# Kernel optimization log

Hardware: AMD Instinct MI355X
Metric: run time of the kernel (lower is better)

## Reference

```python
import math
import jax, jax.numpy as jnp
import numpy as np

B, S, E, H = 4, 2048, 1024, 16
D = E // H


def setup_inputs() -> dict:
    key = jax.random.key(0)
    k1, k2, k3 = jax.random.split(key, 3)
    return {
        "hidden_state": jax.random.normal(k1, (B, S, E), dtype=jnp.float32),
        "attention_mask": jnp.zeros((B, 1, 1, S), dtype=jnp.float32),
        "W_attn": jax.random.normal(k2, (E, 3 * E), dtype=jnp.float32) * 0.02,
        "b_attn": jnp.zeros((3 * E,), dtype=jnp.float32),
        "W_proj": jax.random.normal(k3, (E, E), dtype=jnp.float32) * 0.02,
        "b_proj": jnp.zeros((E,), dtype=jnp.float32),
    }


def reference(hidden_state, attention_mask, W_attn, b_attn, W_proj, b_proj):
    b, s, e = hidden_state.shape
    d = e // H
    # c_attn (HF Conv1D): x @ W + b -> [B,S,3E]
    x = hidden_state @ W_attn + b_attn
    q, k, v = jnp.split(x, 3, axis=-1)
    # split heads -> [B,H,S,D]
    q = q.reshape(b, s, H, d).transpose(0, 2, 1, 3)
    k = k.reshape(b, s, H, d).transpose(0, 2, 1, 3)
    v = v.reshape(b, s, H, d).transpose(0, 2, 1, 3)
    # scores [B,H,S,S]; scale=True divides by sqrt(d_head)
    w = jnp.einsum("bhqd,bhkd->bhqk", q, k) / math.sqrt(d)
    causal = jnp.tril(jnp.ones((s, s), dtype=w.dtype))[None, None]
    w = w * causal + (-10000.0) * (1.0 - causal)
    w = w + attention_mask
    w = jax.nn.softmax(w, axis=-1)  # attn_dropout p=0 (eval)
    out = jnp.einsum("bhqk,bhkd->bhqd", w, v)
    # merge heads -> [B,S,E]
    out = out.transpose(0, 2, 1, 3).reshape(b, s, e)
    # c_proj; resid_dropout p=0 (eval)
    return out @ W_proj + b_proj
```

## Files before the change

### kernel.cpp

```cpp
#include <hip/hip_runtime.h>
#include <hip/hip_bf16.h>

typedef __attribute__((ext_vector_type(4))) float f32x4;
typedef __attribute__((ext_vector_type(8))) short bf16x8;

#define B_SZ  4
#define S_LEN 2048
#define EMB   1024
#define NH    16
#define DH    64
#define E3    3072
#define QKLD  2048
#define LOG2E 1.4426950408889634f
#define SC2   (0.125f * LOG2E)
#define MSTAT 14.0f

__device__ __forceinline__ void gload_lds16(const void* g, void* l) {
  __builtin_amdgcn_global_load_lds((const __attribute__((address_space(1))) void*)g,
                                   (__attribute__((address_space(3))) void*)l, 16, 0, 0);
}

__device__ __forceinline__ float bf2f(unsigned short u) {
  union { unsigned int i; float f; } c;
  c.i = (unsigned int)u << 16;
  return c.f;
}

__global__ void cvt_bf16_kernel(const float* __restrict__ in,
                                __hip_bfloat16* __restrict__ out, int n) {
  const int i = (blockIdx.x * 256 + threadIdx.x) * 4;
  if (i >= n) return;
  const float4 v = *(const float4*)(in + i);
  __align__(8) __hip_bfloat16 o[4];
  o[0] = __float2bfloat16(v.x); o[1] = __float2bfloat16(v.y);
  o[2] = __float2bfloat16(v.z); o[3] = __float2bfloat16(v.w);
  *(uint2*)(out + i) = *(const uint2*)o;
}

__global__ __launch_bounds__(256)
void transpose_cvt(const float* __restrict__ in, __hip_bfloat16* __restrict__ out,
                   int R, int C) {
  __shared__ float tile[32][33];
  const int tx = threadIdx.x & 31, ty = threadIdx.x >> 5;
  const int c = blockIdx.x * 32 + tx;
#pragma unroll
  for (int i = 0; i < 32; i += 8)
    tile[ty + i][tx] = in[(size_t)(blockIdx.y * 32 + ty + i) * C + c];
  __syncthreads();
  const int r2 = blockIdx.y * 32 + tx;
#pragma unroll
  for (int i = 0; i < 32; i += 8)
    out[(size_t)(blockIdx.x * 32 + ty + i) * R + r2] = __float2bfloat16(tile[tx][ty + i]);
}

#define SBAR() { __builtin_amdgcn_s_barrier(); __builtin_amdgcn_sched_barrier(0); }
#define VMCNT(N) asm volatile("s_waitcnt vmcnt(" #N ")" ::: "memory")

#define STG_A(T, H, BUF) { \
    const __hip_bfloat16* s_ = pA + (size_t)((H) * 128) * 1024 + (T) * 64; \
    gload_lds16(s_, (BUF) + (H) * 16384 + w * 1024 + lane * 16); \
    gload_lds16(s_ + 65536, (BUF) + (H) * 16384 + 8192 + w * 1024 + lane * 16); }

#define STG_B(T, H, BUF) { \
    const __hip_bfloat16* s_ = pB + (size_t)((H) * 128) * 1024 + (T) * 64; \
    gload_lds16(s_, (BUF) + (H) * 16384 + w * 1024 + lane * 16); \
    gload_lds16(s_ + 65536, (BUF) + (H) * 16384 + 8192 + w * 1024 + lane * 16); }

#define RD_A(BUF, MH) { _Pragma("unroll") for (int m_ = 0; m_ < 4; ++m_) { \
    a[m_][0] = *(const bf16x8*)((BUF) + arow + ((MH) * 64 + m_ * 16) * 128 + sw0); \
    a[m_][1] = *(const bf16x8*)((BUF) + arow + ((MH) * 64 + m_ * 16) * 128 + sw1); } }

#define RD_B(BUF, NH, BARR) { _Pragma("unroll") for (int n_ = 0; n_ < 2; ++n_) { \
    BARR[n_][0] = *(const bf16x8*)((BUF) + brow + ((NH) * 32 + n_ * 16) * 128 + sw0); \
    BARR[n_][1] = *(const bf16x8*)((BUF) + brow + ((NH) * 32 + n_ * 16) * 128 + sw1); } }

#define MQUAD(MH, NH, BARR) { __builtin_amdgcn_s_setprio(1); \
    _Pragma("unroll") for (int m_ = 0; m_ < 4; ++m_) \
    _Pragma("unroll") for (int n_ = 0; n_ < 2; ++n_) \
    _Pragma("unroll") for (int k_ = 0; k_ < 2; ++k_) \
      acc[(MH)*4+m_][(NH)*2+n_] = __builtin_amdgcn_mfma_f32_16x16x32_bf16( \
          a[m_][k_], BARR[n_][k_], acc[(MH)*4+m_][(NH)*2+n_], 0, 0, 0); \
    __builtin_amdgcn_s_setprio(0); }

template <int EPI>
__global__ __launch_bounds__(512, 2)
void gemm_8ph(const __hip_bfloat16* __restrict__ A, const __hip_bfloat16* __restrict__ BT,
              const float* __restrict__ bias, void* __restrict__ Cout,
              __hip_bfloat16* __restrict__ vt) {
  __shared__ __attribute__((aligned(16))) char lds[131072];
  char* const As0 = lds;
  char* const As1 = lds + 32768;
  char* const Bs0 = lds + 65536;
  char* const Bs1 = lds + 98304;

  const int tid = threadIdx.x;
  const int lane = tid & 63, w = tid >> 6;
  const int lr = lane & 15, lg = lane >> 4, lg4 = lg * 4;
  const int wm = w >> 2, wn = w & 3;
  const int m0 = blockIdx.x * 256, n0 = blockIdx.y * 256;

  const int srl = lane >> 3;
  const int scol = ((lane & 7) ^ srl) * 8;
  const __hip_bfloat16* pA = A + (size_t)(m0 + w * 8 + srl) * 1024 + scol;
  const __hip_bfloat16* pB = BT + (size_t)(n0 + w * 8 + srl) * 1024 + scol;

  const int sw0 = (lg ^ (lr & 7)) << 4;
  const int sw1 = sw0 ^ 0x40;
  const int arow = (wm * 128 + lr) * 128;
  const int brow = (wn * 64 + lr) * 128;

  f32x4 acc[8][4] = {};
  bf16x8 a[4][2], b0[2][2], b1[2][2];

  STG_A(0, 0, As0); STG_B(0, 0, Bs0); STG_A(0, 1, As0); STG_B(0, 1, Bs0); STG_A(1, 0, As1);
  VMCNT(2);
  SBAR();

  auto iter = [&](int t0, bool more) {
    RD_A(As0, 0); RD_B(Bs0, 0, b0);
    STG_B(t0 + 1, 0, Bs1);
    SBAR(); MQUAD(0, 0, b0); SBAR();
    RD_B(Bs0, 1, b1);
    STG_A(t0 + 1, 1, As1);
    SBAR(); MQUAD(0, 1, b1); SBAR();
    RD_A(As0, 1); RD_B(Bs0, 0, b0);
    STG_B(t0 + 1, 1, Bs1);
    SBAR(); MQUAD(1, 0, b0); SBAR();
    RD_B(Bs0, 1, b1);
    if (more) { STG_A(t0 + 2, 0, As0); VMCNT(2); } else { VMCNT(0); }
    SBAR(); MQUAD(1, 1, b1); SBAR();
    RD_A(As1, 0); RD_B(Bs1, 0, b0);
    if (more) STG_B(t0 + 2, 0, Bs0);
    SBAR(); MQUAD(0, 0, b0); SBAR();
    RD_B(Bs1, 1, b1);
    if (more) STG_A(t0 + 2, 1, As0);
    SBAR(); MQUAD(0, 1, b1); SBAR();
    RD_A(As1, 1); RD_B(Bs1, 0, b0);
    if (more) STG_B(t0 + 2, 1, Bs0);
    SBAR(); MQUAD(1, 0, b0); SBAR();
    RD_B(Bs1, 1, b1);
    if (more) { STG_A(t0 + 3, 0, As1); VMCNT(2); }
    SBAR(); MQUAD(1, 1, b1); SBAR();
  };

#pragma unroll 1
  for (int i = 0; i < 7; ++i) iter(2 * i, true);
  iter(14, false);

  if (EPI == 0 && n0 >= 2 * EMB) {
#pragma unroll
    for (int m8 = 0; m8 < 8; ++m8) {
      const int rowg0 = m0 + wm * 128 + m8 * 16 + lg4;
      const int bz = rowg0 >> 11, sloc = rowg0 & (S_LEN - 1);
#pragma unroll
      for (int n4 = 0; n4 < 4; ++n4) {
        const int col = n0 + wn * 64 + n4 * 16 + lr;
        const int c2 = col - 2 * EMB;
        const int hh = c2 >> 6, dd = c2 & 63;
        const float bv = bias[col];
        __align__(8) __hip_bfloat16 pb[4];
#pragma unroll
        for (int r = 0; r < 4; ++r) pb[r] = __float2bfloat16(acc[m8][n4][r] + bv);
        *(uint2*)&vt[(size_t)((bz * NH + hh) * DH + dd) * S_LEN + sloc] = *(const uint2*)pb;
      }
    }
  } else if (EPI == 0) {
#pragma unroll
    for (int m8 = 0; m8 < 8; ++m8) {
#pragma unroll
      for (int n4 = 0; n4 < 4; ++n4) {
        const int col = n0 + wn * 64 + n4 * 16 + lr;
        const float bv = bias[col];
#pragma unroll
        for (int r = 0; r < 4; ++r) {
          const int rowg = m0 + wm * 128 + m8 * 16 + lg4 + r;
          ((__hip_bfloat16*)Cout)[(size_t)rowg * QKLD + col] = __float2bfloat16(acc[m8][n4][r] + bv);
        }
      }
    }
  } else {
#pragma unroll
    for (int m8 = 0; m8 < 8; ++m8) {
#pragma unroll
      for (int n4 = 0; n4 < 4; ++n4) {
        const int col = n0 + wn * 64 + n4 * 16 + lr;
        const float bv = bias[col];
#pragma unroll
        for (int r = 0; r < 4; ++r) {
          const int rowg = m0 + wm * 128 + m8 * 16 + lg4 + r;
          ((float*)Cout)[(size_t)rowg * EMB + col] = acc[m8][n4][r] + bv;
        }
      }
    }
  }
}


template <bool DIAG>
__device__ __forceinline__ void qstep(const char* Ks, const char* Vs,
                                      __hip_bfloat16 (*Psw)[72], const __hip_bfloat16* Msb,
                                      int msoff, const bf16x8 (&aq)[2], f32x4 (&acc)[4],
                                      float& lrun, int lr, int lg, int lg4, int wq) {
  f32x4 sacc[4] = {};
  __builtin_amdgcn_s_setprio(1);
#pragma unroll
  for (int kt = 0; kt < 4; ++kt)
#pragma unroll
    for (int ks = 0; ks < 2; ++ks) {
      const bf16x8 kb = *(const bf16x8*)(Ks + (kt * 16 + lr) * 128 +
                                         (((ks * 4 + lg) ^ (lr & 7)) << 4));
      sacc[kt] = __builtin_amdgcn_mfma_f32_16x16x32_bf16(kb, aq[ks], sacc[kt], 0, 0, 0);
    }
  __builtin_amdgcn_s_setprio(0);
#pragma unroll
  for (int kt = 0; kt < 4; ++kt) {
    const ushort4 mb = *(const ushort4*)&Msb[msoff + kt * 16 + lg4];
    float pp[4];
    __align__(8) __hip_bfloat16 pb[4];
#pragma unroll
    for (int r = 0; r < 4; ++r) {
      float sv = sacc[kt][r] * SC2 + bf2f(((const unsigned short*)&mb)[r]);
      if (DIAG && (kt * 16 + lg4 + r > wq)) sv = -1.0e9f;
      pp[r] = exp2f(sv);
      pb[r] = __float2bfloat16(pp[r]);
    }
    lrun += (pp[0] + pp[1]) + (pp[2] + pp[3]);
    *(uint2*)&Psw[lr][kt * 16 + lg4] = *(const uint2*)pb;
  }
#pragma unroll
  for (int ks = 0; ks < 2; ++ks) {
    const bf16x8 pa = *(const bf16x8*)&Psw[lr][ks * 32 + lg * 8];
    __builtin_amdgcn_s_setprio(1);
#pragma unroll
    for (int dt = 0; dt < 4; ++dt) {
      const bf16x8 vb = *(const bf16x8*)(Vs + (dt * 16 + lr) * 128 +
                                         (((ks * 4 + lg) ^ (lr & 7)) << 4));
      acc[dt] = __builtin_amdgcn_mfma_f32_16x16x32_bf16(pa, vb, acc[dt], 0, 0, 0);
    }
    __builtin_amdgcn_s_setprio(0);
  }
}

template <bool DIAGA>
__device__ __forceinline__ void qstep2(const char* Ks, const char* Vs,
                                       __hip_bfloat16 (*PsA)[72], __hip_bfloat16 (*PsB)[72],
                                       const __hip_bfloat16* Msb, int msoff,
                                       const bf16x8 (&aqA)[2], const bf16x8 (&aqB)[2],
                                       f32x4 (&accA)[4], f32x4 (&accB)[4],
                                       float& lA, float& lB, int lr, int lg, int lg4, int wq) {
  f32x4 sA[4] = {}, sB[4] = {};
  __builtin_amdgcn_s_setprio(1);
#pragma unroll
  for (int kt = 0; kt < 4; ++kt)
#pragma unroll
    for (int ks = 0; ks < 2; ++ks) {
      const bf16x8 kb = *(const bf16x8*)(Ks + (kt * 16 + lr) * 128 +
                                         (((ks * 4 + lg) ^ (lr & 7)) << 4));
      sA[kt] = __builtin_amdgcn_mfma_f32_16x16x32_bf16(kb, aqA[ks], sA[kt], 0, 0, 0);
      sB[kt] = __builtin_amdgcn_mfma_f32_16x16x32_bf16(kb, aqB[ks], sB[kt], 0, 0, 0);
    }
  __builtin_amdgcn_s_setprio(0);
#pragma unroll
  for (int kt = 0; kt < 4; ++kt) {
    const ushort4 mb = *(const ushort4*)&Msb[msoff + kt * 16 + lg4];
    float pA[4], pB[4];
    __align__(8) __hip_bfloat16 bA[4], bB[4];
#pragma unroll
    for (int r = 0; r < 4; ++r) {
      const float mkr = bf2f(((const unsigned short*)&mb)[r]);
      float svA = sA[kt][r] * SC2 + mkr;
      if (DIAGA && (kt * 16 + lg4 + r > wq)) svA = -1.0e9f;
      const float svB = sB[kt][r] * SC2 + mkr;
      pA[r] = exp2f(svA); bA[r] = __float2bfloat16(pA[r]);
      pB[r] = exp2f(svB); bB[r] = __float2bfloat16(pB[r]);
    }
    lA += (pA[0] + pA[1]) + (pA[2] + pA[3]);
    lB += (pB[0] + pB[1]) + (pB[2] + pB[3]);
    *(uint2*)&PsA[lr][kt * 16 + lg4] = *(const uint2*)bA;
    *(uint2*)&PsB[lr][kt * 16 + lg4] = *(const uint2*)bB;
  }
#pragma unroll
  for (int ks = 0; ks < 2; ++ks) {
    const bf16x8 paA = *(const bf16x8*)&PsA[lr][ks * 32 + lg * 8];
    const bf16x8 paB = *(const bf16x8*)&PsB[lr][ks * 32 + lg * 8];
    __builtin_amdgcn_s_setprio(1);
#pragma unroll
    for (int dt = 0; dt < 4; ++dt) {
      const bf16x8 vb = *(const bf16x8*)(Vs + (dt * 16 + lr) * 128 +
                                         (((ks * 4 + lg) ^ (lr & 7)) << 4));
      accA[dt] = __builtin_amdgcn_mfma_f32_16x16x32_bf16(paA, vb, accA[dt], 0, 0, 0);
      accB[dt] = __builtin_amdgcn_mfma_f32_16x16x32_bf16(paB, vb, accB[dt], 0, 0, 0);
    }
    __builtin_amdgcn_s_setprio(0);
  }
}

#define STAGE_LOAD_BUMP()                                                          \
  {                                                                                \
    kpre[0] = *(const bf16x8*)kcur;                                                \
    kpre[1] = *(const bf16x8*)(kcur + 8 * QKLD);                                   \
    vpre[0] = *(const bf16x8*)vcur;                                                \
    vpre[1] = *(const bf16x8*)(vcur + 8 * S_LEN);                                  \
    kcur += 64 * QKLD;                                                             \
    vcur += 64;                                                                    \
  }

#define TILE_SYNC(PREFETCH)                                                        \
  {                                                                                \
    __syncthreads();                                                               \
    *(bf16x8*)kw0 = kpre[0];                                                       \
    *(bf16x8*)(kw0 + 1024) = kpre[1];                                              \
    *(bf16x8*)vw0 = vpre[0];                                                       \
    *(bf16x8*)(vw0 + 1024) = vpre[1];                                              \
    __syncthreads();                                                               \
    if (PREFETCH) STAGE_LOAD_BUMP();                                               \
  }

__global__ __launch_bounds__(256, 4)
void flash_attn8(const __hip_bfloat16* __restrict__ qk, const __hip_bfloat16* __restrict__ vt,
                 const float* __restrict__ amask, __hip_bfloat16* __restrict__ aout) {
  const int j = blockIdx.x;
  const int g = (j & 7) + 8 * (j >> 7);
  const int x = (((j >> 3) & 15) + (((j >> 8) & 3) << 2)) & 15;
  const int h = g >> 2, bz = g & 3;

  const int tid = threadIdx.x;
  const int lane = tid & 63, w = tid >> 6;
  const int lr = lane & 15, lg = lane >> 4, lg4 = lg * 4;
  const int wq = w * 16 + lr;

  const int qta = x, qtb = 31 - x;

  __shared__ __align__(16) __hip_bfloat16 Ks[64 * 64];
  __shared__ __align__(16) __hip_bfloat16 Vs[64 * 64];
  __shared__ __align__(16) __hip_bfloat16 Ps[4][2][16][72];
  __shared__ __align__(8)  __hip_bfloat16 Msb[S_LEN];

  {
    const int e = tid * 8;
    const f32x4 m0v = *(const f32x4*)&amask[bz * S_LEN + e];
    const f32x4 m1v = *(const f32x4*)&amask[bz * S_LEN + e + 4];
    __align__(16) __hip_bfloat16 mb[8];
#pragma unroll
    for (int jj = 0; jj < 4; ++jj) {
      mb[jj]     = __float2bfloat16(m0v[jj] * LOG2E - MSTAT);
      mb[jj + 4] = __float2bfloat16(m1v[jj] * LOG2E - MSTAT);
    }
    *(uint4*)&Msb[e] = *(const uint4*)mb;
  }

  bf16x8 aqA[2], aqB[2];
  {
    const __hip_bfloat16* qpA =
        qk + (size_t)(bz * S_LEN + qta * 64 + w * 16 + lr) * QKLD + h * DH + lg * 8;
    aqA[0] = *(const bf16x8*)qpA; aqA[1] = *(const bf16x8*)(qpA + 32);
    const __hip_bfloat16* qpB =
        qk + (size_t)(bz * S_LEN + qtb * 64 + w * 16 + lr) * QKLD + h * DH + lg * 8;
    aqB[0] = *(const bf16x8*)qpB; aqB[1] = *(const bf16x8*)(qpB + 32);
  }

  f32x4 accA[4] = {}, accB[4] = {};
  float lA = 0.f, lB = 0.f;

  const __hip_bfloat16* kcur = qk + (size_t)bz * S_LEN * QKLD + EMB + h * DH +
                               (size_t)(w * 16 + (lane >> 3)) * QKLD + (lane & 7) * 8;
  const __hip_bfloat16* vcur = vt + (size_t)((bz * NH + h) * DH + w * 16 + (lane >> 3)) * S_LEN +
                               (lane & 7) * 8;
  char* kw0 = (char*)Ks + (w * 16 + (lane >> 3)) * 128 + (((lane & 7) ^ (lane >> 3)) << 4);
  char* vw0 = (char*)Vs + (w * 16 + (lane >> 3)) * 128 + (((lane & 7) ^ (lane >> 3)) << 4);

  bf16x8 kpre[2], vpre[2];
  STAGE_LOAD_BUMP();

  int msoff = 0;
  for (int t = 0; t < qta; ++t) {
    TILE_SYNC(true);
    qstep2<false>((char*)Ks, (char*)Vs, Ps[w][0], Ps[w][1], Msb, msoff,
                  aqA, aqB, accA, accB, lA, lB, lr, lg, lg4, wq);
    msoff += 64;
  }
  TILE_SYNC(true);
  qstep2<true>((char*)Ks, (char*)Vs, Ps[w][0], Ps[w][1], Msb, msoff,
               aqA, aqB, accA, accB, lA, lB, lr, lg, lg4, wq);
  msoff += 64;
  for (int t = qta + 1; t < qtb; ++t) {
    TILE_SYNC(true);
    qstep<false>((char*)Ks, (char*)Vs, Ps[w][1], Msb, msoff, aqB, accB, lB, lr, lg, lg4, wq);
    msoff += 64;
  }
  TILE_SYNC(false);
  qstep<true>((char*)Ks, (char*)Vs, Ps[w][1], Msb, msoff, aqB, accB, lB, lr, lg, lg4, wq);

  lA += __shfl_xor(lA, 16); lA += __shfl_xor(lA, 32);
  lB += __shfl_xor(lB, 16); lB += __shfl_xor(lB, 32);
  float lqA[4], lqB[4];
#pragma unroll
  for (int r = 0; r < 4; ++r) {
    lqA[r] = __shfl(lA, lg4 + r);
    lqB[r] = __shfl(lB, lg4 + r);
  }
#pragma unroll
  for (int dt = 0; dt < 4; ++dt)
#pragma unroll
    for (int r = 0; r < 4; ++r) {
      const int qA = qta * 64 + w * 16 + lg4 + r;
      aout[(size_t)(bz * S_LEN + qA) * EMB + h * DH + dt * 16 + lr] =
          __float2bfloat16(accA[dt][r] / lqA[r]);
      const int qB = qtb * 64 + w * 16 + lg4 + r;
      aout[(size_t)(bz * S_LEN + qB) * EMB + h * DH + dt * 16 + lr] =
          __float2bfloat16(accB[dt][r] / lqB[r]);
    }
}

extern "C" void kernel_launch(void* const* d_in, const int* in_sizes, int n_in,
                              void* d_out, int out_size, void* d_ws, size_t ws_size,
                              hipStream_t stream) {
  const float* hidden = (const float*)d_in[0];
  const float* amask  = (const float*)d_in[1];
  const float* W_attn = (const float*)d_in[2];
  const float* b_attn = (const float*)d_in[3];
  const float* W_proj = (const float*)d_in[4];
  const float* b_proj = (const float*)d_in[5];
  float* out = (float*)d_out;

  char* ws = (char*)d_ws;
  __hip_bfloat16* hbf   = (__hip_bfloat16*)(ws);
  __hip_bfloat16* WaT   = (__hip_bfloat16*)(ws + 16777216);
  __hip_bfloat16* WpT   = (__hip_bfloat16*)(ws + 23068672);
  __hip_bfloat16* qkQK  = (__hip_bfloat16*)(ws + 25165824);
  __hip_bfloat16* vt    = (__hip_bfloat16*)(ws + 58720256);
  __hip_bfloat16* aoutb = (__hip_bfloat16*)(ws + 75497472);

  cvt_bf16_kernel<<<dim3(8192), dim3(256), 0, stream>>>(hidden, hbf, B_SZ * S_LEN * EMB);
  transpose_cvt<<<dim3(96, 32), dim3(256), 0, stream>>>(W_attn, WaT, EMB, E3);
  transpose_cvt<<<dim3(32, 32), dim3(256), 0, stream>>>(W_proj, WpT, EMB, EMB);
  gemm_8ph<0><<<dim3(32, 12), dim3(512), 0, stream>>>(hbf, WaT, b_attn, qkQK, vt);
  flash_attn8<<<dim3(1024), dim3(256), 0, stream>>>(qkQK, vt, amask, aoutb);
  gemm_8ph<1><<<dim3(32, 4), dim3(512), 0, stream>>>(aoutb, WpT, b_proj, out, nullptr);
}
```

Baseline: 187.9 us.

## Rewrite GEMM as triple-buffered K32 pipeline and cheapen softmax exp/packing

The GEMM's 8-phase double-buffered K64 schedule is replaced by a simpler three-stage LDS ring of K32 tiles. Each stage is loaded two steps ahead with direct global-to-LDS loads, and one raw barrier per step replaces the many phase barriers. In the attention kernel, exp2f becomes the hardware exp2 intrinsic and bf16 packing of P uses truncation instead of round-to-nearest, cutting VALU work. The price is slightly lower precision in P, and the GEMM's prefetch depth per barrier and barrier count change.

```diff
diff --git a/kernel.cpp b/kernel.cpp
--- a/kernel.cpp
+++ b/kernel.cpp
@@ -15,6 +15,9 @@
 #define SC2   (0.125f * LOG2E)
 #define MSTAT 14.0f
 
+#define VMCNT(N) asm volatile("s_waitcnt vmcnt(" #N ")" ::: "memory")
+#define RAWBAR() asm volatile("s_barrier" ::: "memory")
+
 __device__ __forceinline__ void gload_lds16(const void* g, void* l) {
   __builtin_amdgcn_global_load_lds((const __attribute__((address_space(1))) void*)g,
                                    (__attribute__((address_space(3))) void*)l, 16, 0, 0);
@@ -24,6 +27,12 @@
   union { unsigned int i; float f; } c;
   c.i = (unsigned int)u << 16;
   return c.f;
+}
+
+__device__ __forceinline__ unsigned pack_bf16_rtz(float hi, float lo) {
+  union { float f; unsigned u; } a, b;
+  a.f = hi; b.f = lo;
+  return (a.u & 0xffff0000u) | (b.u >> 16);
 }
 
 __global__ void cvt_bf16_kernel(const float* __restrict__ in,
@@ -53,99 +62,67 @@
     out[(size_t)(blockIdx.x * 32 + ty + i) * R + r2] = __float2bfloat16(tile[tx][ty + i]);
 }
 
-#define SBAR() { __builtin_amdgcn_s_barrier(); __builtin_amdgcn_sched_barrier(0); }
-#define VMCNT(N) asm volatile("s_waitcnt vmcnt(" #N ")" ::: "memory")
-
-#define STG_A(T, H, BUF) { \
-    const __hip_bfloat16* s_ = pA + (size_t)((H) * 128) * 1024 + (T) * 64; \
-    gload_lds16(s_, (BUF) + (H) * 16384 + w * 1024 + lane * 16); \
-    gload_lds16(s_ + 65536, (BUF) + (H) * 16384 + 8192 + w * 1024 + lane * 16); }
-
-#define STG_B(T, H, BUF) { \
-    const __hip_bfloat16* s_ = pB + (size_t)((H) * 128) * 1024 + (T) * 64; \
-    gload_lds16(s_, (BUF) + (H) * 16384 + w * 1024 + lane * 16); \
-    gload_lds16(s_ + 65536, (BUF) + (H) * 16384 + 8192 + w * 1024 + lane * 16); }
-
-#define RD_A(BUF, MH) { _Pragma("unroll") for (int m_ = 0; m_ < 4; ++m_) { \
-    a[m_][0] = *(const bf16x8*)((BUF) + arow + ((MH) * 64 + m_ * 16) * 128 + sw0); \
-    a[m_][1] = *(const bf16x8*)((BUF) + arow + ((MH) * 64 + m_ * 16) * 128 + sw1); } }
-
-#define RD_B(BUF, NH, BARR) { _Pragma("unroll") for (int n_ = 0; n_ < 2; ++n_) { \
-    BARR[n_][0] = *(const bf16x8*)((BUF) + brow + ((NH) * 32 + n_ * 16) * 128 + sw0); \
-    BARR[n_][1] = *(const bf16x8*)((BUF) + brow + ((NH) * 32 + n_ * 16) * 128 + sw1); } }
-
-#define MQUAD(MH, NH, BARR) { __builtin_amdgcn_s_setprio(1); \
-    _Pragma("unroll") for (int m_ = 0; m_ < 4; ++m_) \
-    _Pragma("unroll") for (int n_ = 0; n_ < 2; ++n_) \
-    _Pragma("unroll") for (int k_ = 0; k_ < 2; ++k_) \
-      acc[(MH)*4+m_][(NH)*2+n_] = __builtin_amdgcn_mfma_f32_16x16x32_bf16( \
-          a[m_][k_], BARR[n_][k_], acc[(MH)*4+m_][(NH)*2+n_], 0, 0, 0); \
-    __builtin_amdgcn_s_setprio(0); }
-
 template <int EPI>
 __global__ __launch_bounds__(512, 2)
-void gemm_8ph(const __hip_bfloat16* __restrict__ A, const __hip_bfloat16* __restrict__ BT,
-              const float* __restrict__ bias, void* __restrict__ Cout,
-              __hip_bfloat16* __restrict__ vt) {
-  __shared__ __attribute__((aligned(16))) char lds[131072];
-  char* const As0 = lds;
-  char* const As1 = lds + 32768;
-  char* const Bs0 = lds + 65536;
-  char* const Bs1 = lds + 98304;
-
+void gemm_v3(const __hip_bfloat16* __restrict__ A, const __hip_bfloat16* __restrict__ BT,
+             const float* __restrict__ bias, void* __restrict__ Cout,
+             __hip_bfloat16* __restrict__ vt) {
+  __shared__ __attribute__((aligned(16))) char lds[98304];
   const int tid = threadIdx.x;
   const int lane = tid & 63, w = tid >> 6;
   const int lr = lane & 15, lg = lane >> 4, lg4 = lg * 4;
   const int wm = w >> 2, wn = w & 3;
   const int m0 = blockIdx.x * 256, n0 = blockIdx.y * 256;
 
-  const int srl = lane >> 3;
-  const int scol = ((lane & 7) ^ srl) * 8;
-  const __hip_bfloat16* pA = A + (size_t)(m0 + w * 8 + srl) * 1024 + scol;
-  const __hip_bfloat16* pB = BT + (size_t)(n0 + w * 8 + srl) * 1024 + scol;
-
-  const int sw0 = (lg ^ (lr & 7)) << 4;
-  const int sw1 = sw0 ^ 0x40;
-  const int arow = (wm * 128 + lr) * 128;
-  const int brow = (wn * 64 + lr) * 128;
+  const int srow = tid >> 2;
+  const int scol = ((tid & 3) ^ ((tid >> 3) & 3)) << 3;
+  const __hip_bfloat16* pA = A + (size_t)(m0 + srow) * 1024 + scol;
+  const __hip_bfloat16* pB = BT + (size_t)(n0 + srow) * 1024 + scol;
+  char* const ldsd = lds + tid * 16;
+
+  const int sw = (lg ^ ((lr >> 1) & 3)) << 4;
+  const int abyte = (wm * 128 + lr) * 64 + sw;
+  const int bbyte = 16384 + (wn * 64 + lr) * 64 + sw;
 
   f32x4 acc[8][4] = {};
-  bf16x8 a[4][2], b0[2][2], b1[2][2];
-
-  STG_A(0, 0, As0); STG_B(0, 0, Bs0); STG_A(0, 1, As0); STG_B(0, 1, Bs0); STG_A(1, 0, As1);
-  VMCNT(2);
-  SBAR();
-
-  auto iter = [&](int t0, bool more) {
-    RD_A(As0, 0); RD_B(Bs0, 0, b0);
-    STG_B(t0 + 1, 0, Bs1);
-    SBAR(); MQUAD(0, 0, b0); SBAR();
-    RD_B(Bs0, 1, b1);
-    STG_A(t0 + 1, 1, As1);
-    SBAR(); MQUAD(0, 1, b1); SBAR();
-    RD_A(As0, 1); RD_B(Bs0, 0, b0);
-    STG_B(t0 + 1, 1, Bs1);
-    SBAR(); MQUAD(1, 0, b0); SBAR();
-    RD_B(Bs0, 1, b1);
-    if (more) { STG_A(t0 + 2, 0, As0); VMCNT(2); } else { VMCNT(0); }
-    SBAR(); MQUAD(1, 1, b1); SBAR();
-    RD_A(As1, 0); RD_B(Bs1, 0, b0);
-    if (more) STG_B(t0 + 2, 0, Bs0);
-    SBAR(); MQUAD(0, 0, b0); SBAR();
-    RD_B(Bs1, 1, b1);
-    if (more) STG_A(t0 + 2, 1, As0);
-    SBAR(); MQUAD(0, 1, b1); SBAR();
-    RD_A(As1, 1); RD_B(Bs1, 0, b0);
-    if (more) STG_B(t0 + 2, 1, Bs0);
-    SBAR(); MQUAD(1, 0, b0); SBAR();
-    RD_B(Bs1, 1, b1);
-    if (more) { STG_A(t0 + 3, 0, As1); VMCNT(2); }
-    SBAR(); MQUAD(1, 1, b1); SBAR();
-  };
-
+
+  gload_lds16(pA,                 ldsd);
+  gload_lds16(pA + 131072,        ldsd + 8192);
+  gload_lds16(pB,                 ldsd + 16384);
+  gload_lds16(pB + 131072,        ldsd + 24576);
+  gload_lds16(pA + 32,            ldsd + 32768);
+  gload_lds16(pA + 131072 + 32,   ldsd + 32768 + 8192);
+  gload_lds16(pB + 32,            ldsd + 32768 + 16384);
+  gload_lds16(pB + 131072 + 32,   ldsd + 32768 + 24576);
+
+  int cur = 0;
 #pragma unroll 1
-  for (int i = 0; i < 7; ++i) iter(2 * i, true);
-  iter(14, false);
+  for (int t = 0; t < 32; ++t) {
+    if (t < 31) { VMCNT(4); } else { VMCNT(0); }
+    RAWBAR();
+    if (t + 2 < 32) {
+      const int nb = (cur >= 1) ? cur - 1 : 2;
+      char* d = ldsd + nb * 32768;
+      const __hip_bfloat16* sa = pA + (t + 2) * 32;
+      const __hip_bfloat16* sb = pB + (t + 2) * 32;
+      gload_lds16(sa,          d);
+      gload_lds16(sa + 131072, d + 8192);
+      gload_lds16(sb,          d + 16384);
+      gload_lds16(sb + 131072, d + 24576);
+    }
+    const char* base = lds + cur * 32768;
+    bf16x8 a[8], b[4];
+#pragma unroll
+    for (int m = 0; m < 8; ++m) a[m] = *(const bf16x8*)(base + abyte + m * 1024);
+#pragma unroll
+    for (int n = 0; n < 4; ++n) b[n] = *(const bf16x8*)(base + bbyte + n * 1024);
+#pragma unroll
+    for (int m = 0; m < 8; ++m)
+#pragma unroll
+      for (int n = 0; n < 4; ++n)
+        acc[m][n] = __builtin_amdgcn_mfma_f32_16x16x32_bf16(a[m], b[n], acc[m][n], 0, 0, 0);
+    cur = (cur == 2) ? 0 : cur + 1;
+  }
 
   if (EPI == 0 && n0 >= 2 * EMB) {
 #pragma unroll
@@ -194,7 +171,6 @@
     }
   }
 }
-
 
 template <bool DIAG>
 __device__ __forceinline__ void qstep(const char* Ks, const char* Vs,
@@ -216,16 +192,17 @@
   for (int kt = 0; kt < 4; ++kt) {
     const ushort4 mb = *(const ushort4*)&Msb[msoff + kt * 16 + lg4];
     float pp[4];
-    __align__(8) __hip_bfloat16 pb[4];
 #pragma unroll
     for (int r = 0; r < 4; ++r) {
       float sv = sacc[kt][r] * SC2 + bf2f(((const unsigned short*)&mb)[r]);
       if (DIAG && (kt * 16 + lg4 + r > wq)) sv = -1.0e9f;
-      pp[r] = exp2f(sv);
-      pb[r] = __float2bfloat16(pp[r]);
+      pp[r] = __builtin_amdgcn_exp2f(sv);
     }
     lrun += (pp[0] + pp[1]) + (pp[2] + pp[3]);
-    *(uint2*)&Psw[lr][kt * 16 + lg4] = *(const uint2*)pb;
+    uint2 uu;
+    uu.x = pack_bf16_rtz(pp[1], pp[0]);
+    uu.y = pack_bf16_rtz(pp[3], pp[2]);
+    *(uint2*)&Psw[lr][kt * 16 + lg4] = uu;
   }
 #pragma unroll
   for (int ks = 0; ks < 2; ++ks) {
@@ -264,20 +241,24 @@
   for (int kt = 0; kt < 4; ++kt) {
     const ushort4 mb = *(const ushort4*)&Msb[msoff + kt * 16 + lg4];
     float pA[4], pB[4];
-    __align__(8) __hip_bfloat16 bA[4], bB[4];
 #pragma unroll
     for (int r = 0; r < 4; ++r) {
       const float mkr = bf2f(((const unsigned short*)&mb)[r]);
       float svA = sA[kt][r] * SC2 + mkr;
       if (DIAGA && (kt * 16 + lg4 + r > wq)) svA = -1.0e9f;
       const float svB = sB[kt][r] * SC2 + mkr;
-      pA[r] = exp2f(svA); bA[r] = __float2bfloat16(pA[r]);
-      pB[r] = exp2f(svB); bB[r] = __float2bfloat16(pB[r]);
+      pA[r] = __builtin_amdgcn_exp2f(svA);
+      pB[r] = __builtin_amdgcn_exp2f(svB);
     }
     lA += (pA[0] + pA[1]) + (pA[2] + pA[3]);
     lB += (pB[0] + pB[1]) + (pB[2] + pB[3]);
-    *(uint2*)&PsA[lr][kt * 16 + lg4] = *(const uint2*)bA;
-    *(uint2*)&PsB[lr][kt * 16 + lg4] = *(const uint2*)bB;
+    uint2 ua, ub;
+    ua.x = pack_bf16_rtz(pA[1], pA[0]);
+    ua.y = pack_bf16_rtz(pA[3], pA[2]);
+    ub.x = pack_bf16_rtz(pB[1], pB[0]);
+    ub.y = pack_bf16_rtz(pB[3], pB[2]);
+    *(uint2*)&PsA[lr][kt * 16 + lg4] = ua;
+    *(uint2*)&PsB[lr][kt * 16 + lg4] = ub;
   }
 #pragma unroll
   for (int ks = 0; ks < 2; ++ks) {
@@ -317,8 +298,8 @@
   }
 
 __global__ __launch_bounds__(256, 4)
-void flash_attn8(const __hip_bfloat16* __restrict__ qk, const __hip_bfloat16* __restrict__ vt,
-                 const float* __restrict__ amask, __hip_bfloat16* __restrict__ aout) {
+void flash_attn10(const __hip_bfloat16* __restrict__ qk, const __hip_bfloat16* __restrict__ vt,
+                  const float* __restrict__ amask, __hip_bfloat16* __restrict__ aout) {
   const int j = blockIdx.x;
   const int g = (j & 7) + 8 * (j >> 7);
   const int x = (((j >> 3) & 15) + (((j >> 8) & 3) << 2)) & 15;
@@ -434,7 +415,7 @@
   cvt_bf16_kernel<<<dim3(8192), dim3(256), 0, stream>>>(hidden, hbf, B_SZ * S_LEN * EMB);
   transpose_cvt<<<dim3(96, 32), dim3(256), 0, stream>>>(W_attn, WaT, EMB, E3);
   transpose_cvt<<<dim3(32, 32), dim3(256), 0, stream>>>(W_proj, WpT, EMB, EMB);
-  gemm_8ph<0><<<dim3(32, 12), dim3(512), 0, stream>>>(hbf, WaT, b_attn, qkQK, vt);
-  flash_attn8<<<dim3(1024), dim3(256), 0, stream>>>(qkQK, vt, amask, aoutb);
-  gemm_8ph<1><<<dim3(32, 4), dim3(512), 0, stream>>>(aoutb, WpT, b_proj, out, nullptr);
-}
+  gemm_v3<0><<<dim3(32, 12), dim3(512), 0, stream>>>(hbf, WaT, b_attn, qkQK, vt);
+  flash_attn10<<<dim3(1024), dim3(256), 0, stream>>>(qkQK, vt, amask, aoutb);
+  gemm_v3<1><<<dim3(32, 4), dim3(512), 0, stream>>>(aoutb, WpT, b_proj, out, nullptr);
+}
```

Measured after the change: 183.9 us. -2.1%, faster.
